# Performance work log

Hardware: AMD Instinct MI355X
Metric: run time of the kernel (lower is better)

Reference implementation:

```python
import jax, jax.numpy as jnp
import numpy as np
import math

B, S, D = 1, 4096, 512
H, KVH, DH = 8, 4, 64
DH2 = DH // 2
M = int(math.isqrt(S))           # product-key grid side, S == M*M
K = 8                            # top_k
ROPE_BASE = 10000.0


def rope_cos_sin(seq_len, dh, base):
    inv_freq = 1.0 / (base ** (jnp.arange(0, dh, 2, dtype=jnp.float32) / dh))
    t = jnp.arange(seq_len, dtype=jnp.float32)
    freqs = jnp.outer(t, inv_freq)                      # (S, dh/2)
    emb = jnp.concatenate([freqs, freqs], axis=-1)      # (S, dh)
    return jnp.cos(emb), jnp.sin(emb)


def apply_rope(x, cos, sin):
    # x: (B, H, S, dh); half-split rotation (llama-style)
    dh2 = x.shape[-1] // 2
    rot = jnp.concatenate([-x[..., dh2:], x[..., :dh2]], axis=-1)
    return x * cos + rot * sin


def setup_inputs() -> dict:
    key = jax.random.key(0)
    ks = jax.random.split(key, 5)
    s = 0.02
    x = jax.random.normal(ks[0], (B, S, D), dtype=jnp.float32)
    Wq = jax.random.normal(ks[1], (H * DH, D), dtype=jnp.float32) * s
    Wk = jax.random.normal(ks[2], (KVH * DH, D), dtype=jnp.float32) * s
    Wv = jax.random.normal(ks[3], (KVH * DH, D), dtype=jnp.float32) * s
    Wo = jax.random.normal(ks[4], (D, H * DH), dtype=jnp.float32) * s
    return {"x": x, "Wq": Wq, "Wk": Wk, "Wv": Wv, "Wo": Wo}


def reference(x, Wq, Wk, Wv, Wo):
    b, s, d = x.shape
    cos, sin = rope_cos_sin(s, DH, ROPE_BASE)
    q = (x @ Wq.T).reshape(b, s, H, DH).transpose(0, 2, 1, 3)      # (B,H,S,DH)
    k = (x @ Wk.T).reshape(b, s, KVH, DH).transpose(0, 2, 1, 3)    # (B,KVH,S,DH)
    v = (x @ Wv.T).reshape(b, s, KVH, DH).transpose(0, 2, 1, 3)
    q = apply_rope(q, cos, sin)
    k = apply_rope(k, cos, sin)
    rep = H // KVH                                                 # GQA repeat_kv
    k = jnp.repeat(k, rep, axis=1)                                 # (B,H,S,DH)
    v = jnp.repeat(v, rep, axis=1)

    # factorized product keys: sum over grid rows / cols
    kg = k.reshape(b, H, M, M, DH)
    k1 = kg[..., :DH2].sum(axis=-2)                                # (B,H,M,DH2)
    k2 = kg[..., DH2:].sum(axis=-3)                                # (B,H,M,DH2)
    q1, q2 = q[..., :DH2], q[..., DH2:]

    def topk_sel(qh, kh):  # qh: (S,DH2), kh: (M,DH2)
        scores = qh @ kh.T                                         # (S,M)
        _, idx = jax.lax.top_k(scores, K)                          # (S,K)
        return kh[idx], idx                                        # (S,K,DH2), (S,K)

    sel2 = jax.vmap(jax.vmap(topk_sel))
    k1v, i1 = sel2(q1, k1)                                         # (B,H,S,K,DH2)
    k2v, i2 = sel2(q2, k2)

    # cross-product candidates: (B,H,S,K,K,DH) -> (B,H,S,K*K,DH)
    c1 = jnp.broadcast_to(k1v[:, :, :, :, None, :], (b, H, s, K, K, DH2))
    c2 = jnp.broadcast_to(k2v[:, :, :, None, :, :], (b, H, s, K, K, DH2))
    cand = jnp.concatenate([c1, c2], axis=-1).reshape(b, H, s, K * K, DH)

    scores_final = jnp.einsum('bhsd,bhscd->bhsc', q, cand)         # (B,H,S,K*K)
    _, sel = jax.lax.top_k(scores_final, K)                        # (B,H,S,K)
    final_k = jnp.take_along_axis(cand, sel[..., None], axis=3)    # (B,H,S,K,DH)

    row = jnp.take_along_axis(i1, sel // K, axis=3)
    col = jnp.take_along_axis(i2, sel % K, axis=3)
    v_idx = row * M + col                                          # (B,H,S,K)
    final_v = jax.vmap(jax.vmap(lambda vb, ib: vb[ib]))(v, v_idx)  # (B,H,S,K,DH)

    attn = jax.nn.softmax(
        jnp.einsum('bhsd,bhskd->bhsk', q, final_k) / math.sqrt(DH), axis=-1)
    o = jnp.einsum('bhsk,bhskd->bhsd', attn, final_v)              # (B,H,S,DH)
    o = o.transpose(0, 2, 1, 3).reshape(b, s, H * DH)
    return o @ Wo.T
```

## Files before the change

kernel.cpp:

```cpp
#include <hip/hip_runtime.h>
#include <math.h>


static constexpr size_t OFF_QKV = 0;
static constexpr size_t OFF_Q   = 4194304;
static constexpr size_t OFF_K   = 6291456;
static constexpr size_t OFF_V   = 7340032;
static constexpr size_t OFF_COS = 8388608;
static constexpr size_t OFF_SIN = 8519680;
static constexpr size_t OFF_K1  = 8650752;
static constexpr size_t OFF_K2  = 8658944;
static constexpr size_t OFF_O   = 8667136;
static constexpr size_t OFF_W   = 10764288;

#define LDT 68

__device__ __forceinline__ float rdlane_f(float v, int lane) {
  return __int_as_float(__builtin_amdgcn_readlane(__float_as_int(v), lane));
}

__global__ __launch_bounds__(256) void freq_table_kernel(float* __restrict__ cosT,
    float* __restrict__ sinT) {
  int idx = blockIdx.x * 256 + threadIdx.x;
  int s = idx >> 5;
  int dp = idx & 31;
  double e = (double)dp * (1.0 / 32.0);
  float pf = (float)pow(10000.0, e);
  float invf = 1.0f / pf;
  float argf = __fmul_rn((float)s, invf);
  cosT[idx] = (float)cos((double)argf);
  sinT[idx] = (float)sin((double)argf);
}

template <int SPLIT>
__global__ __launch_bounds__(256) void gemm_nt_chain(const float* __restrict__ A,
    const float* __restrict__ B, float* __restrict__ C, int N) {
  __shared__ float As[16 * LDT];
  __shared__ float Bs[16 * LDT];
  const int tid = threadIdx.x;
  const int ty = tid >> 4;
  const int tx = tid & 15;
  const int bm = blockIdx.y, bn = blockIdx.x;
  const int lrow = tid >> 2;
  const int lk = (tid & 3) << 2;
  const float* Ap = A + (size_t)(bm * 64 + lrow) * 512 + lk;
  const float* Bp = B + (size_t)(bn * 64 + lrow) * 512 + lk;
  float acc1[4][4] = {{0.f}};
  float acc2[4][4] = {{0.f}};
  for (int kt = 0; kt < 512; kt += 16) {
    float4 av = *(const float4*)(Ap + kt);
    float4 bv = *(const float4*)(Bp + kt);
    __syncthreads();
    As[(lk + 0) * LDT + lrow] = av.x;
    As[(lk + 1) * LDT + lrow] = av.y;
    As[(lk + 2) * LDT + lrow] = av.z;
    As[(lk + 3) * LDT + lrow] = av.w;
    Bs[(lk + 0) * LDT + lrow] = bv.x;
    Bs[(lk + 1) * LDT + lrow] = bv.y;
    Bs[(lk + 2) * LDT + lrow] = bv.z;
    Bs[(lk + 3) * LDT + lrow] = bv.w;
    __syncthreads();
    if (SPLIT != 0 && kt >= SPLIT) {
      #pragma unroll
      for (int k = 0; k < 16; ++k) {
        float4 a4 = *(const float4*)(&As[k * LDT + (ty << 2)]);
        float4 b4 = *(const float4*)(&Bs[k * LDT + (tx << 2)]);
        float af[4] = {a4.x, a4.y, a4.z, a4.w};
        float bf[4] = {b4.x, b4.y, b4.z, b4.w};
        #pragma unroll
        for (int i2 = 0; i2 < 4; ++i2)
          #pragma unroll
          for (int j2 = 0; j2 < 4; ++j2)
            acc2[i2][j2] = fmaf(af[i2], bf[j2], acc2[i2][j2]);
      }
    } else {
      #pragma unroll
      for (int k = 0; k < 16; ++k) {
        float4 a4 = *(const float4*)(&As[k * LDT + (ty << 2)]);
        float4 b4 = *(const float4*)(&Bs[k * LDT + (tx << 2)]);
        float af[4] = {a4.x, a4.y, a4.z, a4.w};
        float bf[4] = {b4.x, b4.y, b4.z, b4.w};
        #pragma unroll
        for (int i2 = 0; i2 < 4; ++i2)
          #pragma unroll
          for (int j2 = 0; j2 < 4; ++j2)
            acc1[i2][j2] = fmaf(af[i2], bf[j2], acc1[i2][j2]);
      }
    }
  }
  float* Cp = C + (size_t)(bm * 64 + (ty << 2)) * N + bn * 64 + (tx << 2);
  #pragma unroll
  for (int i2 = 0; i2 < 4; ++i2) {
    float4 o4;
    o4.x = __fadd_rn(acc1[i2][0], acc2[i2][0]);
    o4.y = __fadd_rn(acc1[i2][1], acc2[i2][1]);
    o4.z = __fadd_rn(acc1[i2][2], acc2[i2][2]);
    o4.w = __fadd_rn(acc1[i2][3], acc2[i2][3]);
    *(float4*)(Cp + (size_t)i2 * N) = o4;
  }
}

__global__ __launch_bounds__(256) void rope_reshape_kernel(const float* __restrict__ raw,
    const float* __restrict__ cosT, const float* __restrict__ sinT,
    float* __restrict__ qb, float* __restrict__ kb, float* __restrict__ vb) {
  int idx = blockIdx.x * 256 + threadIdx.x;
  int s = idx >> 10;
  int n = idx & 1023;
  float val = raw[idx];
  int d = n & 63;
  if (n < 768) {
    int dp = d & 31;
    float cs = cosT[(s << 5) + dp];
    float sn = sinT[(s << 5) + dp];
    int npart = (n - d) + ((d < 32) ? d + 32 : d - 32);
    float partner = raw[(s << 10) + npart];
    float rot = (d < 32) ? -partner : partner;
    float out = __fadd_rn(__fmul_rn(val, cs), __fmul_rn(rot, sn));
    if (n < 512) {
      int h = n >> 6;
      qb[((size_t)(h * 4096 + s) << 6) + d] = out;
    } else {
      int kvh = (n - 512) >> 6;
      kb[((size_t)(kvh * 4096 + s) << 6) + d] = out;
    }
  } else {
    int kvh = (n - 768) >> 6;
    vb[((size_t)(kvh * 4096 + s) << 6) + d] = val;
  }
}

__global__ __launch_bounds__(256) void k12_np_kernel(const float* __restrict__ kb,
    float* __restrict__ k1t, float* __restrict__ k2t) {
  int id = blockIdx.x * 256 + threadIdx.x;
  int which = id >> 13;
  int rem = id & 8191;
  int kvh = rem >> 11;
  int rem2 = rem & 2047;
  int i = rem2 >> 5;
  int d = rem2 & 31;
  const float* base = kb + ((size_t)(kvh * 4096) << 6);
  if (which == 0) {
    float acc = base[((size_t)(i * 64) << 6) + d];
    for (int c = 1; c < 64; ++c)
      acc = __fadd_rn(acc, base[((size_t)(i * 64 + c) << 6) + d]);
    k1t[(kvh * 64 + i) * 32 + d] = acc;
  } else {
    float acc = base[((size_t)i << 6) + d + 32];
    for (int r = 1; r < 64; ++r)
      acc = __fadd_rn(acc, base[((size_t)(r * 64 + i) << 6) + d + 32]);
    k2t[(kvh * 64 + i) * 32 + d] = acc;
  }
}

__global__ __launch_bounds__(256) void stage1_scores_kernel(
    const float* __restrict__ qb, const float* __restrict__ k1t,
    const float* __restrict__ k2t, float* __restrict__ sc) {
  __shared__ float qs[64 * 68];
  __shared__ float kd[32 * 132];
  const int t = threadIdx.x;
  const int h = blockIdx.y;
  const int s0 = blockIdx.x * 64;
  const int kvh = h >> 1;
  #pragma unroll
  for (int i = 0; i < 16; ++i) {
    int j = t + i * 256;
    int ss = j >> 6, d = j & 63;
    qs[d * 68 + ss] = qb[((size_t)(h * 4096 + s0 + ss) << 6) + d];
  }
  #pragma unroll
  for (int i = 0; i < 8; ++i) {
    int j = t + i * 256;
    int r = j >> 5, d = j & 31;
    kd[d * 132 + r]      = k1t[(kvh * 64 + r) * 32 + d];
    kd[d * 132 + 64 + r] = k2t[(kvh * 64 + r) * 32 + d];
  }
  __syncthreads();
  const int ty = t >> 4;
  const int tx = t & 15;
  const int qrow = (tx >= 8) ? 32 : 0;
  float acc[4][8] = {{0.f}};
  #pragma unroll
  for (int d = 0; d < 32; ++d) {
    float4 a4 = *(const float4*)&qs[(qrow + d) * 68 + (ty << 2)];
    float4 b0 = *(const float4*)&kd[d * 132 + (tx << 3)];
    float4 b1 = *(const float4*)&kd[d * 132 + (tx << 3) + 4];
    float af[4] = {a4.x, a4.y, a4.z, a4.w};
    float bf[8] = {b0.x, b0.y, b0.z, b0.w, b1.x, b1.y, b1.z, b1.w};
    #pragma unroll
    for (int i2 = 0; i2 < 4; ++i2)
      #pragma unroll
      for (int j2 = 0; j2 < 8; ++j2)
        acc[i2][j2] = fmaf(af[i2], bf[j2], acc[i2][j2]);
  }
  #pragma unroll
  for (int i2 = 0; i2 < 4; ++i2) {
    float* p = sc + (((size_t)(h * 4096 + s0 + (ty << 2) + i2)) << 7) + (tx << 3);
    *(float4*)(p)     = make_float4(acc[i2][0], acc[i2][1], acc[i2][2], acc[i2][3]);
    *(float4*)(p + 4) = make_float4(acc[i2][4], acc[i2][5], acc[i2][6], acc[i2][7]);
  }
}

__device__ __forceinline__ void bitonic64_val_desc(float& v, int lane) {
  #pragma unroll
  for (int k = 2; k <= 64; k <<= 1) {
    #pragma unroll
    for (int j = k >> 1; j >= 1; j >>= 1) {
      float ov = __shfl_xor(v, j, 64);
      bool up = ((lane & k) == 0) == ((lane & j) == 0);
      float mx = fmaxf(v, ov), mn = fminf(v, ov);
      v = up ? mx : mn;
    }
  }
}

__global__ __launch_bounds__(256) void attn_sel_kernel(const float* __restrict__ sc,
    const float* __restrict__ qb, const float* __restrict__ vb,
    const float* __restrict__ k1t, const float* __restrict__ k2t,
    float* __restrict__ ob) {
  const int lane = threadIdx.x & 63;
  const int w = blockIdx.x * 4 + (threadIdx.x >> 6);
  const int h = w >> 12;
  const int s = w & 4095;
  const int kvh = h >> 1;
  const float* scp = sc + ((size_t)w << 7);
  const float s1 = scp[lane];
  const float s2 = scp[64 + lane];
  const float qv = qb[((size_t)w << 6) + lane];

  float v1 = s1;
  bitonic64_val_desc(v1, lane);
  unsigned long long pack1 = 0, used = 0;
  #pragma unroll
  for (int t = 0; t < 8; ++t) {
    float tv = rdlane_f(v1, t);
    unsigned long long m = __ballot(s1 == tv) & ~used;
    int ix = __ffsll((long long)m) - 1;
    used |= 1ull << ix;
    pack1 |= (unsigned long long)ix << (6 * t);
  }
  float v2 = s2;
  bitonic64_val_desc(v2, lane);
  unsigned long long pack2 = 0;
  used = 0;
  #pragma unroll
  for (int t = 0; t < 8; ++t) {
    float tv = rdlane_f(v2, t);
    unsigned long long m = __ballot(s2 == tv) & ~used;
    int ix = __ffsll((long long)m) - 1;
    used |= 1ull << ix;
    pack2 |= (unsigned long long)ix << (6 * t);
  }

  int r1 = (int)((pack1 >> (6 * (lane >> 3))) & 63);
  int r2 = (int)((pack2 >> (6 * (lane & 7))) & 63);
  const float* k1p = k1t + (size_t)(kvh * 64 + r1) * 32;
  const float* k2p = k2t + (size_t)(kvh * 64 + r2) * 32;
  float c = 0.f;
  #pragma unroll
  for (int dq = 0; dq < 32; dq += 4) {
    float4 kk = *(const float4*)(k1p + dq);
    c = __fadd_rn(c, __fmul_rn(rdlane_f(qv, dq + 0), kk.x));
    c = __fadd_rn(c, __fmul_rn(rdlane_f(qv, dq + 1), kk.y));
    c = __fadd_rn(c, __fmul_rn(rdlane_f(qv, dq + 2), kk.z));
    c = __fadd_rn(c, __fmul_rn(rdlane_f(qv, dq + 3), kk.w));
  }
  #pragma unroll
  for (int dq = 0; dq < 32; dq += 4) {
    float4 kk = *(const float4*)(k2p + dq);
    c = __fadd_rn(c, __fmul_rn(rdlane_f(qv, 32 + dq + 0), kk.x));
    c = __fadd_rn(c, __fmul_rn(rdlane_f(qv, 32 + dq + 1), kk.y));
    c = __fadd_rn(c, __fmul_rn(rdlane_f(qv, 32 + dq + 2), kk.z));
    c = __fadd_rn(c, __fmul_rn(rdlane_f(qv, 32 + dq + 3), kk.w));
  }
  const float scand = c;
  float v3 = c;
  bitonic64_val_desc(v3, lane);
  float cvs[8]; int ccs[8];
  used = 0;
  #pragma unroll
  for (int t = 0; t < 8; ++t) {
    float tv = rdlane_f(v3, t);
    unsigned long long m = __ballot(scand == tv) & ~used;
    int ix = __ffsll((long long)m) - 1;
    used |= 1ull << ix;
    cvs[t] = tv;
    ccs[t] = ix;
  }
  float y[8];
  #pragma unroll
  for (int t = 0; t < 8; ++t) y[t] = cvs[t] * 0.125f;
  float mx = y[0];
  #pragma unroll
  for (int t = 1; t < 8; ++t) if (y[t] > mx) mx = y[t];
  float e[8];
  #pragma unroll
  for (int t = 0; t < 8; ++t) e[t] = __expf(__fsub_rn(y[t], mx));
  float wsum = __fadd_rn(__fadd_rn(__fadd_rn(e[0], e[1]), __fadd_rn(e[2], e[3])),
                         __fadd_rn(__fadd_rn(e[4], e[5]), __fadd_rn(e[6], e[7])));
  const float* vbh = vb + ((size_t)kvh << 18);
  float o = 0.f;
  #pragma unroll
  for (int t = 0; t < 8; ++t) {
    float att = __fdiv_rn(e[t], wsum);
    int row = (int)((pack1 >> (6 * (ccs[t] >> 3))) & 63);
    int col = (int)((pack2 >> (6 * (ccs[t] & 7))) & 63);
    o = __fadd_rn(o, __fmul_rn(att, vbh[((size_t)(row * 64 + col) << 6) + lane]));
  }
  ob[(size_t)s * 512 + (h << 6) + lane] = o;
}

extern "C" void kernel_launch(void* const* d_in, const int* in_sizes, int n_in,
                              void* d_out, int out_size, void* d_ws, size_t ws_size,
                              hipStream_t stream) {
  const float* x  = (const float*)d_in[0];
  const float* Wq = (const float*)d_in[1];
  const float* Wk = (const float*)d_in[2];
  const float* Wv = (const float*)d_in[3];
  const float* Wo = (const float*)d_in[4];
  float* ws = (float*)d_ws;
  float* qkv  = ws + OFF_QKV;
  float* qb   = ws + OFF_Q;
  float* kb   = ws + OFF_K;
  float* vb   = ws + OFF_V;
  float* cosT = ws + OFF_COS;
  float* sinT = ws + OFF_SIN;
  float* k1t  = ws + OFF_K1;
  float* k2t  = ws + OFF_K2;
  float* ob   = ws + OFF_O;
  float* wcat = ws + OFF_W;
  float* scb  = ws + OFF_QKV;

  hipMemcpyAsync(wcat,             Wq, (size_t)512 * 512 * sizeof(float), hipMemcpyDeviceToDevice, stream);
  hipMemcpyAsync(wcat + 512 * 512, Wk, (size_t)256 * 512 * sizeof(float), hipMemcpyDeviceToDevice, stream);
  hipMemcpyAsync(wcat + 768 * 512, Wv, (size_t)256 * 512 * sizeof(float), hipMemcpyDeviceToDevice, stream);

  freq_table_kernel<<<512, 256, 0, stream>>>(cosT, sinT);
  gemm_nt_chain<384><<<dim3(1024 / 64, 4096 / 64), 256, 0, stream>>>(x, wcat, qkv, 1024);
  rope_reshape_kernel<<<16384, 256, 0, stream>>>(qkv, cosT, sinT, qb, kb, vb);
  k12_np_kernel<<<64, 256, 0, stream>>>(kb, k1t, k2t);
  stage1_scores_kernel<<<dim3(64, 8), 256, 0, stream>>>(qb, k1t, k2t, scb);
  attn_sel_kernel<<<8192, 256, 0, stream>>>(scb, qb, vb, k1t, k2t, ob);
  gemm_nt_chain<0><<<dim3(512 / 64, 4096 / 64), 256, 0, stream>>>(ob, Wo, (float*)d_out, 512);
}
```

Baseline: 246.6 us.

## Enlarge SGEMM tiles to 128x128 with 8x8 per-thread outputs and register prefetch

Both projection GEMMs now use 128x128 block tiles with an 8x8 register micro-tile per thread instead of 64x64 with 4x4. The next k-slice is loaded from global memory into registers while the current slice is being computed. This raises arithmetic intensity per shared-memory load and hides global load latency. In exchange register pressure roughly quadruples (two 64-float accumulator arrays in the split variant) and the grid drops to 256 and 128 blocks, which could leave the GPU's CUs underfilled.

Measured after the change: 278.4 us. +12.9%, slower.

```diff
diff --git a/kernel.cpp b/kernel.cpp
--- a/kernel.cpp
+++ b/kernel.cpp
@@ -13,7 +13,7 @@
 static constexpr size_t OFF_O   = 8667136;
 static constexpr size_t OFF_W   = 10764288;
 
-#define LDT 68
+#define LDB 132
 
 __device__ __forceinline__ float rdlane_f(float v, int lane) {
   return __int_as_float(__builtin_amdgcn_readlane(__float_as_int(v), lane));
@@ -33,70 +33,100 @@
 }
 
 template <int SPLIT>
-__global__ __launch_bounds__(256) void gemm_nt_chain(const float* __restrict__ A,
+__global__ __launch_bounds__(256) void gemm128_chain(const float* __restrict__ A,
     const float* __restrict__ B, float* __restrict__ C, int N) {
-  __shared__ float As[16 * LDT];
-  __shared__ float Bs[16 * LDT];
+  __shared__ float As[16 * LDB];
+  __shared__ float Bs[16 * LDB];
   const int tid = threadIdx.x;
+  const int bm = blockIdx.y, bn = blockIdx.x;
+  const int lrow = tid >> 1;
+  const int lko = (tid & 1) << 3;
   const int ty = tid >> 4;
   const int tx = tid & 15;
-  const int bm = blockIdx.y, bn = blockIdx.x;
-  const int lrow = tid >> 2;
-  const int lk = (tid & 3) << 2;
-  const float* Ap = A + (size_t)(bm * 64 + lrow) * 512 + lk;
-  const float* Bp = B + (size_t)(bn * 64 + lrow) * 512 + lk;
-  float acc1[4][4] = {{0.f}};
-  float acc2[4][4] = {{0.f}};
+  const float* Ap = A + (size_t)(bm * 128 + lrow) * 512 + lko;
+  const float* Bp = B + (size_t)(bn * 128 + lrow) * 512 + lko;
+  float acc1[8][8] = {{0.f}};
+  float acc2[8][8] = {{0.f}};
+  float4 a0 = *(const float4*)(Ap + 0);
+  float4 a1 = *(const float4*)(Ap + 4);
+  float4 b0 = *(const float4*)(Bp + 0);
+  float4 b1 = *(const float4*)(Bp + 4);
   for (int kt = 0; kt < 512; kt += 16) {
-    float4 av = *(const float4*)(Ap + kt);
-    float4 bv = *(const float4*)(Bp + kt);
     __syncthreads();
-    As[(lk + 0) * LDT + lrow] = av.x;
-    As[(lk + 1) * LDT + lrow] = av.y;
-    As[(lk + 2) * LDT + lrow] = av.z;
-    As[(lk + 3) * LDT + lrow] = av.w;
-    Bs[(lk + 0) * LDT + lrow] = bv.x;
-    Bs[(lk + 1) * LDT + lrow] = bv.y;
-    Bs[(lk + 2) * LDT + lrow] = bv.z;
-    Bs[(lk + 3) * LDT + lrow] = bv.w;
+    As[(lko + 0) * LDB + lrow] = a0.x;
+    As[(lko + 1) * LDB + lrow] = a0.y;
+    As[(lko + 2) * LDB + lrow] = a0.z;
+    As[(lko + 3) * LDB + lrow] = a0.w;
+    As[(lko + 4) * LDB + lrow] = a1.x;
+    As[(lko + 5) * LDB + lrow] = a1.y;
+    As[(lko + 6) * LDB + lrow] = a1.z;
+    As[(lko + 7) * LDB + lrow] = a1.w;
+    Bs[(lko + 0) * LDB + lrow] = b0.x;
+    Bs[(lko + 1) * LDB + lrow] = b0.y;
+    Bs[(lko + 2) * LDB + lrow] = b0.z;
+    Bs[(lko + 3) * LDB + lrow] = b0.w;
+    Bs[(lko + 4) * LDB + lrow] = b1.x;
+    Bs[(lko + 5) * LDB + lrow] = b1.y;
+    Bs[(lko + 6) * LDB + lrow] = b1.z;
+    Bs[(lko + 7) * LDB + lrow] = b1.w;
     __syncthreads();
+    if (kt + 16 < 512) {
+      a0 = *(const float4*)(Ap + kt + 16);
+      a1 = *(const float4*)(Ap + kt + 20);
+      b0 = *(const float4*)(Bp + kt + 16);
+      b1 = *(const float4*)(Bp + kt + 20);
+    }
     if (SPLIT != 0 && kt >= SPLIT) {
       #pragma unroll
       for (int k = 0; k < 16; ++k) {
-        float4 a4 = *(const float4*)(&As[k * LDT + (ty << 2)]);
-        float4 b4 = *(const float4*)(&Bs[k * LDT + (tx << 2)]);
-        float af[4] = {a4.x, a4.y, a4.z, a4.w};
-        float bf[4] = {b4.x, b4.y, b4.z, b4.w};
+        float4 al = *(const float4*)(&As[k * LDB + (ty << 3)]);
+        float4 ah = *(const float4*)(&As[k * LDB + (ty << 3) + 4]);
+        float4 bl = *(const float4*)(&Bs[k * LDB + (tx << 3)]);
+        float4 bh = *(const float4*)(&Bs[k * LDB + (tx << 3) + 4]);
+        float af[8] = {al.x, al.y, al.z, al.w, ah.x, ah.y, ah.z, ah.w};
+        float bf[8] = {bl.x, bl.y, bl.z, bl.w, bh.x, bh.y, bh.z, bh.w};
         #pragma unroll
-        for (int i2 = 0; i2 < 4; ++i2)
+        for (int i2 = 0; i2 < 8; ++i2)
           #pragma unroll
-          for (int j2 = 0; j2 < 4; ++j2)
+          for (int j2 = 0; j2 < 8; ++j2)
             acc2[i2][j2] = fmaf(af[i2], bf[j2], acc2[i2][j2]);
       }
     } else {
       #pragma unroll
       for (int k = 0; k < 16; ++k) {
-        float4 a4 = *(const float4*)(&As[k * LDT + (ty << 2)]);
-        float4 b4 = *(const float4*)(&Bs[k * LDT + (tx << 2)]);
-        float af[4] = {a4.x, a4.y, a4.z, a4.w};
-        float bf[4] = {b4.x, b4.y, b4.z, b4.w};
+        float4 al = *(const float4*)(&As[k * LDB + (ty << 3)]);
+        float4 ah = *(const float4*)(&As[k * LDB + (ty << 3) + 4]);
+        float4 bl = *(const float4*)(&Bs[k * LDB + (tx << 3)]);
+        float4 bh = *(const float4*)(&Bs[k * LDB + (tx << 3) + 4]);
+        float af[8] = {al.x, al.y, al.z, al.w, ah.x, ah.y, ah.z, ah.w};
+        float bf[8] = {bl.x, bl.y, bl.z, bl.w, bh.x, bh.y, bh.z, bh.w};
         #pragma unroll
-        for (int i2 = 0; i2 < 4; ++i2)
+        for (int i2 = 0; i2 < 8; ++i2)
           #pragma unroll
-          for (int j2 = 0; j2 < 4; ++j2)
+          for (int j2 = 0; j2 < 8; ++j2)
             acc1[i2][j2] = fmaf(af[i2], bf[j2], acc1[i2][j2]);
       }
     }
   }
-  float* Cp = C + (size_t)(bm * 64 + (ty << 2)) * N + bn * 64 + (tx << 2);
-  #pragma unroll
-  for (int i2 = 0; i2 < 4; ++i2) {
-    float4 o4;
-    o4.x = __fadd_rn(acc1[i2][0], acc2[i2][0]);
-    o4.y = __fadd_rn(acc1[i2][1], acc2[i2][1]);
-    o4.z = __fadd_rn(acc1[i2][2], acc2[i2][2]);
-    o4.w = __fadd_rn(acc1[i2][3], acc2[i2][3]);
-    *(float4*)(Cp + (size_t)i2 * N) = o4;
+  #pragma unroll
+  for (int i2 = 0; i2 < 8; ++i2) {
+    float* Cp = C + (size_t)(bm * 128 + (ty << 3) + i2) * N + bn * 128 + (tx << 3);
+    float4 lo, hi;
+    if (SPLIT != 0) {
+      lo.x = __fadd_rn(acc1[i2][0], acc2[i2][0]);
+      lo.y = __fadd_rn(acc1[i2][1], acc2[i2][1]);
+      lo.z = __fadd_rn(acc1[i2][2], acc2[i2][2]);
+      lo.w = __fadd_rn(acc1[i2][3], acc2[i2][3]);
+      hi.x = __fadd_rn(acc1[i2][4], acc2[i2][4]);
+      hi.y = __fadd_rn(acc1[i2][5], acc2[i2][5]);
+      hi.z = __fadd_rn(acc1[i2][6], acc2[i2][6]);
+      hi.w = __fadd_rn(acc1[i2][7], acc2[i2][7]);
+    } else {
+      lo = make_float4(acc1[i2][0], acc1[i2][1], acc1[i2][2], acc1[i2][3]);
+      hi = make_float4(acc1[i2][4], acc1[i2][5], acc1[i2][6], acc1[i2][7]);
+    }
+    *(float4*)(Cp)     = lo;
+    *(float4*)(Cp + 4) = hi;
   }
 }
 
@@ -335,10 +365,10 @@
   hipMemcpyAsync(wcat + 768 * 512, Wv, (size_t)256 * 512 * sizeof(float), hipMemcpyDeviceToDevice, stream);
 
   freq_table_kernel<<<512, 256, 0, stream>>>(cosT, sinT);
-  gemm_nt_chain<384><<<dim3(1024 / 64, 4096 / 64), 256, 0, stream>>>(x, wcat, qkv, 1024);
+  gemm128_chain<384><<<dim3(1024 / 128, 4096 / 128), 256, 0, stream>>>(x, wcat, qkv, 1024);
   rope_reshape_kernel<<<16384, 256, 0, stream>>>(qkv, cosT, sinT, qb, kb, vb);
   k12_np_kernel<<<64, 256, 0, stream>>>(kb, k1t, k2t);
   stage1_scores_kernel<<<dim3(64, 8), 256, 0, stream>>>(qb, k1t, k2t, scb);
   attn_sel_kernel<<<8192, 256, 0, stream>>>(scb, qb, vb, k1t, k2t, ob);
-  gemm_nt_chain<0><<<dim3(512 / 64, 4096 / 64), 256, 0, stream>>>(ob, Wo, (float*)d_out, 512);
-}
+  gemm128_chain<0><<<dim3(512 / 128, 4096 / 128), 256, 0, stream>>>(ob, Wo, (float*)d_out, 512);
+}
```
